# Performance work log

Measured on AMD Instinct MI355X. Metric: run time of the kernel, lower is better.

## Reference

```python
import jax, jax.numpy as jnp
import numpy as np

B, L, E, Q = 32, 2048, 512, 512

def setup_inputs() -> dict:
    key = jax.random.key(0)
    k1, k2, k3, k4, k5 = jax.random.split(key, 5)
    scale_attn = 1.0 / np.sqrt(E + Q)
    scale_v = 1.0 / np.sqrt(E)
    return {
        "embeddings": jax.random.normal(k1, (B, L, E), dtype=jnp.float32),
        "query": jax.random.normal(k2, (B, L, Q), dtype=jnp.float32),
        "W_attn": jax.random.normal(k3, (E, E + Q), dtype=jnp.float32) * scale_attn,
        "b_attn": jax.random.normal(k4, (E,), dtype=jnp.float32) * scale_attn,
        "v_w": jax.random.normal(k5, (E,), dtype=jnp.float32) * scale_v,
    }

def reference(embeddings, query, W_attn, b_attn, v_w):
    # concat along feature dim: (B, L, Q+E)
    cat = jnp.concatenate([query, embeddings], axis=2)
    # attn_layer: Linear(E+Q -> E), then tanh: (B, L, E)
    h = jnp.tanh(jnp.einsum('blf,ef->ble', cat, W_attn) + b_attn)
    # attn_v: Linear(E -> 1, no bias) -> scores (B, L)
    scores = jnp.einsum('ble,e->bl', h, v_w)
    # softmax over the sequence (dim=1 in torch)
    w = jax.nn.softmax(scores, axis=1)  # (B, L)
    # transpose to (B, 1, L) then bmm with embeddings -> (B, 1, E)
    applied = jnp.einsum('bl,ble->be', w, embeddings)[:, None, :]
    weights = w[:, None, :]
    return (applied, weights)
```

## Files before the change

kernel.cpp:

```cpp
#include <hip/hip_runtime.h>
#include <hip/hip_bf16.h>
#include <math.h>


typedef __attribute__((ext_vector_type(8))) short bf16x8;
typedef __attribute__((ext_vector_type(4))) float f32x4;

#define BDIM 32
#define LDIM 2048
#define EDIM 512
#define QDIM 512
#define KDIM 1024
#define MDIM (BDIM * LDIM)

#define BM 128
#define BN 128
#define BK 64
#define NSTEPS (KDIM / BK)

#define BAR() do { \
    asm volatile("s_waitcnt vmcnt(8) lgkmcnt(0)" ::: "memory"); \
    __builtin_amdgcn_s_barrier(); \
    __builtin_amdgcn_sched_barrier(0); \
} while (0)

__device__ __forceinline__ unsigned int pack2bf(float lo, float hi) {
    unsigned int a = __builtin_bit_cast(unsigned int, lo) + 0x8000u;
    unsigned int b = __builtin_bit_cast(unsigned int, hi) + 0x8000u;
    return __builtin_amdgcn_perm(b, a, 0x07060302);
}

__global__ __launch_bounds__(256) void convert_w_kernel(
    const float* __restrict__ W, unsigned short* __restrict__ Wsw)
{
    const int gid = blockIdx.x * 256 + threadIdx.x;
    const int n  = gid >> 7;
    const int jb = (gid & 127) * 16;
    const int sb = jb ^ ((n & 7) << 4);
    const float* src = W + (size_t)n * KDIM + (sb >> 1);
    const float4 a = *(const float4*)(src);
    const float4 c = *(const float4*)(src + 4);
    uint4 o;
    o.x = pack2bf(a.x, a.y); o.y = pack2bf(a.z, a.w);
    o.z = pack2bf(c.x, c.y); o.w = pack2bf(c.z, c.w);
    *(uint4*)((char*)Wsw + (size_t)n * 2048 + jb) = o;
}

__device__ __forceinline__ bf16x8 lds_frag(const unsigned short* buf, int row, int cb) {
    return *(const bf16x8*)((const char*)buf + row * 128 + (cb ^ ((row & 7) << 4)));
}

__device__ __forceinline__ void load_a(const float* __restrict__ emb,
                                       const float* __restrict__ query,
                                       int m0, int kstep, int arow, int acol,
                                       float4 (&r)[8])
{
    const int k0 = kstep * BK;
    const float* asrc = (k0 < QDIM) ? query : emb;
    const int koff = (k0 < QDIM) ? k0 : (k0 - QDIM);
    #pragma unroll
    for (int p = 0; p < 8; p++)
        r[p] = *(const float4*)(asrc + (size_t)(m0 + p * 16 + arow) * 512 + koff + acol);
}

__device__ __forceinline__ void write_a(unsigned short* buf, int arow, int acolb,
                                        int axor, const float4 (&r)[8])
{
    #pragma unroll
    for (int p = 0; p < 8; p++) {
        uint2 pk;
        pk.x = pack2bf(r[p].x, r[p].y);
        pk.y = pack2bf(r[p].z, r[p].w);
        *(uint2*)((char*)buf + (p * 16 + arow) * 128 + (acolb ^ axor)) = pk;
    }
}

__device__ __forceinline__ void gll_b(const unsigned short* __restrict__ Wsw,
                                      unsigned short* buf, int n0, int kstep,
                                      int brow, int bcb, int wvoff)
{
    const size_t kb = (size_t)kstep * (BK * 2);
    #pragma unroll
    for (int p = 0; p < 4; p++) {
        const char* g = (const char*)Wsw + (size_t)(n0 + p * 32 + brow) * 2048 + kb + bcb;
        __builtin_amdgcn_global_load_lds(
            (const __attribute__((address_space(1))) void*)g,
            (__attribute__((address_space(3))) void*)((char*)buf + p * 4096 + wvoff),
            16, 0, 0);
    }
}

__device__ __forceinline__ void compute_step(const unsigned short* a_,
                                             const unsigned short* b_,
                                             int wm, int wn, int ln, int quad,
                                             f32x4 (&acc)[4][4])
{
    __builtin_amdgcn_s_setprio(1);
    #pragma unroll
    for (int ks = 0; ks < 2; ks++) {
        bf16x8 af[4], bfr[4];
        #pragma unroll
        for (int i = 0; i < 4; i++) af[i] = lds_frag(a_, wm + i * 16 + ln, ks * 64 + quad * 16);
        #pragma unroll
        for (int j = 0; j < 4; j++) bfr[j] = lds_frag(b_, wn + j * 16 + ln, ks * 64 + quad * 16);
        #pragma unroll
        for (int i = 0; i < 4; i++)
            #pragma unroll
            for (int j = 0; j < 4; j++)
                acc[i][j] = __builtin_amdgcn_mfma_f32_16x16x32_bf16(af[i], bfr[j], acc[i][j], 0, 0, 0);
    }
    __builtin_amdgcn_s_setprio(0);
}

__global__ __launch_bounds__(256, 2) void scores_kernel(
    const float* __restrict__ emb, const float* __restrict__ query,
    const unsigned short* __restrict__ Wsw, const float* __restrict__ b_attn,
    const float* __restrict__ v_w, float* __restrict__ part)
{
    __shared__ __align__(16) unsigned short As[2][BM * BK];
    __shared__ __align__(16) unsigned short Bs[2][BN * BK];

    const int tid = threadIdx.x;
    const int bid = blockIdx.x;
    const int xcd = bid & 7;
    const int slot = bid >> 3;
    const int mtile = xcd * 64 + (slot >> 2);
    const int ntile = slot & 3;
    const int m0 = mtile * BM;
    const int n0 = ntile * BN;

    const int lane = tid & 63;
    const int wv = tid >> 6;
    const int wm = (wv >> 1) * 64;
    const int wn = (wv & 1) * 64;
    const int quad = lane >> 4;
    const int ln = lane & 15;

    const int arow  = tid >> 4;
    const int acol  = (tid & 15) * 4;
    const int acolb = acol * 2;
    const int axor  = (arow & 7) << 4;

    const int brow = tid >> 3;
    const int bcb  = (tid & 7) * 16;
    const int wvoff = __builtin_amdgcn_readfirstlane((tid >> 6) << 10);

    f32x4 acc[4][4];
    #pragma unroll
    for (int i = 0; i < 4; i++)
        #pragma unroll
        for (int j = 0; j < 4; j++)
            acc[i][j] = (f32x4){0.f, 0.f, 0.f, 0.f};

    float4 ra[8], rb[8];

    load_a(emb, query, m0, 0, arow, acol, ra);
    gll_b(Wsw, &Bs[0][0], n0, 0, brow, bcb, wvoff);
    load_a(emb, query, m0, 1, arow, acol, rb);
    write_a(&As[0][0], arow, acolb, axor, ra);
    BAR();

    for (int t = 0; t < NSTEPS; t += 2) {
        gll_b(Wsw, &Bs[1][0], n0, t + 1, brow, bcb, wvoff);
        {
            const int kpre = (t + 2 < NSTEPS) ? t + 2 : NSTEPS - 1;
            load_a(emb, query, m0, kpre, arow, acol, ra);
        }
        write_a(&As[1][0], arow, acolb, axor, rb);
        compute_step(&As[0][0], &Bs[0][0], wm, wn, ln, quad, acc);
        BAR();

        {
            const int kst = (t + 2 < NSTEPS) ? t + 2 : NSTEPS - 1;
            gll_b(Wsw, &Bs[0][0], n0, kst, brow, bcb, wvoff);
            const int kpre = (t + 3 < NSTEPS) ? t + 3 : NSTEPS - 1;
            load_a(emb, query, m0, kpre, arow, acol, rb);
            write_a(&As[0][0], arow, acolb, axor, ra);
        }
        compute_step(&As[1][0], &Bs[1][0], wm, wn, ln, quad, acc);
        BAR();
    }

    float bj[4], vj[4];
    #pragma unroll
    for (int j = 0; j < 4; j++) {
        const int n = n0 + wn + j * 16 + ln;
        bj[j] = b_attn[n];
        vj[j] = v_w[n];
    }
    float* redbuf = (float*)&As[0][0];
    const int half = wn >> 6;
    #pragma unroll
    for (int i = 0; i < 4; i++) {
        #pragma unroll
        for (int r = 0; r < 4; r++) {
            float s = 0.f;
            #pragma unroll
            for (int j = 0; j < 4; j++)
                s += tanhf(acc[i][j][r] + bj[j]) * vj[j];
            #pragma unroll
            for (int off = 1; off < 16; off <<= 1)
                s += __shfl_xor(s, off, 64);
            if (ln == 0)
                redbuf[half * 128 + wm + i * 16 + quad * 4 + r] = s;
        }
    }
    __syncthreads();
    if (tid < 128)
        part[(size_t)ntile * MDIM + m0 + tid] = redbuf[tid] + redbuf[128 + tid];
}

__global__ __launch_bounds__(256) void softmax_stats_kernel(
    const float* __restrict__ part, float* __restrict__ out_weights)
{
    const int b = blockIdx.x;
    const int tid = threadIdx.x;
    __shared__ float red[4];

    float sv[8];
    #pragma unroll
    for (int t = 0; t < 8; t++) {
        const size_t idx = (size_t)b * LDIM + tid + t * 256;
        float s = part[idx];
        #pragma unroll
        for (int j = 1; j < 4; j++) s += part[(size_t)j * MDIM + idx];
        sv[t] = s;
    }

    float mx = sv[0];
    #pragma unroll
    for (int t = 1; t < 8; t++) mx = fmaxf(mx, sv[t]);
    #pragma unroll
    for (int off = 1; off < 64; off <<= 1) mx = fmaxf(mx, __shfl_xor(mx, off, 64));
    if ((tid & 63) == 0) red[tid >> 6] = mx;
    __syncthreads();
    mx = fmaxf(fmaxf(red[0], red[1]), fmaxf(red[2], red[3]));

    float sm = 0.f;
    #pragma unroll
    for (int t = 0; t < 8; t++) sm += expf(sv[t] - mx);
    #pragma unroll
    for (int off = 1; off < 64; off <<= 1) sm += __shfl_xor(sm, off, 64);
    __syncthreads();
    if ((tid & 63) == 0) red[tid >> 6] = sm;
    __syncthreads();
    sm = red[0] + red[1] + red[2] + red[3];
    const float inv = 1.f / sm;

    #pragma unroll
    for (int t = 0; t < 8; t++)
        out_weights[(size_t)b * LDIM + tid + t * 256] = expf(sv[t] - mx) * inv;
}

__global__ __launch_bounds__(256) void apply_kernel(
    const float* __restrict__ emb, const float* __restrict__ w,
    float* __restrict__ out_applied)
{
    const int b = blockIdx.x >> 6;
    const int chunk = blockIdx.x & 63;
    const int l0 = chunk * 32;
    const int tid = threadIdx.x;

    __shared__ float wls[32];
    __shared__ float partial[512];

    if (tid < 32) wls[tid] = w[(size_t)b * LDIM + l0 + tid];
    __syncthreads();

    const int half = tid >> 7;
    const int cg = tid & 127;
    float4 acc = {0.f, 0.f, 0.f, 0.f};
    const float* ebase = emb + ((size_t)b * LDIM + l0 + half) * EDIM + cg * 4;
    #pragma unroll
    for (int i = 0; i < 16; i++) {
        const float4 v = *(const float4*)(ebase + (size_t)2 * i * EDIM);
        const float ww = wls[half + 2 * i];
        acc.x += ww * v.x;
        acc.y += ww * v.y;
        acc.z += ww * v.z;
        acc.w += ww * v.w;
    }
    if (half == 1) *(float4*)&partial[cg * 4] = acc;
    __syncthreads();
    if (half == 0) {
        const float4 p = *(const float4*)&partial[cg * 4];
        float* dst = out_applied + (size_t)b * EDIM + cg * 4;
        atomicAdd(dst + 0, acc.x + p.x);
        atomicAdd(dst + 1, acc.y + p.y);
        atomicAdd(dst + 2, acc.z + p.z);
        atomicAdd(dst + 3, acc.w + p.w);
    }
}

extern "C" void kernel_launch(void* const* d_in, const int* in_sizes, int n_in,
                              void* d_out, int out_size, void* d_ws, size_t ws_size,
                              hipStream_t stream) {
    const float* emb    = (const float*)d_in[0];
    const float* query  = (const float*)d_in[1];
    const float* W      = (const float*)d_in[2];
    const float* b_attn = (const float*)d_in[3];
    const float* v_w    = (const float*)d_in[4];

    float* out     = (float*)d_out;
    float* applied = out;
    float* weights = out + BDIM * EDIM;

    float* part = (float*)d_ws;
    unsigned short* Wsw = (unsigned short*)((char*)d_ws + (size_t)4 * MDIM * 4);

    hipMemsetAsync(applied, 0, (size_t)BDIM * EDIM * sizeof(float), stream);

    convert_w_kernel<<<256, 256, 0, stream>>>(W, Wsw);

    scores_kernel<<<2048, 256, 0, stream>>>(emb, query, Wsw, b_attn, v_w, part);

    softmax_stats_kernel<<<32, 256, 0, stream>>>(part, weights);

    apply_kernel<<<2048, 256, 0, stream>>>(emb, weights, applied);
}
```

Before: 392.1 us.

## Load GEMM fragments directly from global memory into registers, bypassing LDS

The LDS-staged, double-buffered tiling of A and B is replaced by per-wave loads straight into registers, with two register chunk buffers alternating in a loop. The W conversion no longer swizzles and writes plain row-major bf16. This removes LDS traffic and barriers, but each wave now fetches its own A and B fragments with no sharing across waves. That raises global and L2 traffic, and the small strided loads leave less latency hiding.

```diff
diff --git a/kernel.cpp b/kernel.cpp
--- a/kernel.cpp
+++ b/kernel.cpp
@@ -15,14 +15,7 @@
 
 #define BM 128
 #define BN 128
-#define BK 64
-#define NSTEPS (KDIM / BK)
-
-#define BAR() do { \
-    asm volatile("s_waitcnt vmcnt(8) lgkmcnt(0)" ::: "memory"); \
-    __builtin_amdgcn_s_barrier(); \
-    __builtin_amdgcn_sched_barrier(0); \
-} while (0)
+#define NCHUNK 32
 
 __device__ __forceinline__ unsigned int pack2bf(float lo, float hi) {
     unsigned int a = __builtin_bit_cast(unsigned int, lo) + 0x8000u;
@@ -30,95 +23,68 @@
     return __builtin_amdgcn_perm(b, a, 0x07060302);
 }
 
+__device__ __forceinline__ bf16x8 pack_frag(const float4& lo, const float4& hi) {
+    union { unsigned int u[4]; bf16x8 v; } r;
+    r.u[0] = pack2bf(lo.x, lo.y);
+    r.u[1] = pack2bf(lo.z, lo.w);
+    r.u[2] = pack2bf(hi.x, hi.y);
+    r.u[3] = pack2bf(hi.z, hi.w);
+    return r.v;
+}
+
 __global__ __launch_bounds__(256) void convert_w_kernel(
-    const float* __restrict__ W, unsigned short* __restrict__ Wsw)
+    const float* __restrict__ W, unsigned short* __restrict__ Wbf)
 {
     const int gid = blockIdx.x * 256 + threadIdx.x;
-    const int n  = gid >> 7;
-    const int jb = (gid & 127) * 16;
-    const int sb = jb ^ ((n & 7) << 4);
-    const float* src = W + (size_t)n * KDIM + (sb >> 1);
+    const float* src = W + (size_t)gid * 8;
     const float4 a = *(const float4*)(src);
     const float4 c = *(const float4*)(src + 4);
     uint4 o;
     o.x = pack2bf(a.x, a.y); o.y = pack2bf(a.z, a.w);
     o.z = pack2bf(c.x, c.y); o.w = pack2bf(c.z, c.w);
-    *(uint4*)((char*)Wsw + (size_t)n * 2048 + jb) = o;
-}
-
-__device__ __forceinline__ bf16x8 lds_frag(const unsigned short* buf, int row, int cb) {
-    return *(const bf16x8*)((const char*)buf + row * 128 + (cb ^ ((row & 7) << 4)));
-}
-
-__device__ __forceinline__ void load_a(const float* __restrict__ emb,
-                                       const float* __restrict__ query,
-                                       int m0, int kstep, int arow, int acol,
-                                       float4 (&r)[8])
-{
-    const int k0 = kstep * BK;
-    const float* asrc = (k0 < QDIM) ? query : emb;
-    const int koff = (k0 < QDIM) ? k0 : (k0 - QDIM);
-    #pragma unroll
-    for (int p = 0; p < 8; p++)
-        r[p] = *(const float4*)(asrc + (size_t)(m0 + p * 16 + arow) * 512 + koff + acol);
-}
-
-__device__ __forceinline__ void write_a(unsigned short* buf, int arow, int acolb,
-                                        int axor, const float4 (&r)[8])
-{
-    #pragma unroll
-    for (int p = 0; p < 8; p++) {
-        uint2 pk;
-        pk.x = pack2bf(r[p].x, r[p].y);
-        pk.y = pack2bf(r[p].z, r[p].w);
-        *(uint2*)((char*)buf + (p * 16 + arow) * 128 + (acolb ^ axor)) = pk;
-    }
-}
-
-__device__ __forceinline__ void gll_b(const unsigned short* __restrict__ Wsw,
-                                      unsigned short* buf, int n0, int kstep,
-                                      int brow, int bcb, int wvoff)
-{
-    const size_t kb = (size_t)kstep * (BK * 2);
-    #pragma unroll
-    for (int p = 0; p < 4; p++) {
-        const char* g = (const char*)Wsw + (size_t)(n0 + p * 32 + brow) * 2048 + kb + bcb;
-        __builtin_amdgcn_global_load_lds(
-            (const __attribute__((address_space(1))) void*)g,
-            (__attribute__((address_space(3))) void*)((char*)buf + p * 4096 + wvoff),
-            16, 0, 0);
-    }
-}
-
-__device__ __forceinline__ void compute_step(const unsigned short* a_,
-                                             const unsigned short* b_,
-                                             int wm, int wn, int ln, int quad,
-                                             f32x4 (&acc)[4][4])
-{
-    __builtin_amdgcn_s_setprio(1);
-    #pragma unroll
-    for (int ks = 0; ks < 2; ks++) {
-        bf16x8 af[4], bfr[4];
-        #pragma unroll
-        for (int i = 0; i < 4; i++) af[i] = lds_frag(a_, wm + i * 16 + ln, ks * 64 + quad * 16);
-        #pragma unroll
-        for (int j = 0; j < 4; j++) bfr[j] = lds_frag(b_, wn + j * 16 + ln, ks * 64 + quad * 16);
-        #pragma unroll
-        for (int i = 0; i < 4; i++)
-            #pragma unroll
-            for (int j = 0; j < 4; j++)
-                acc[i][j] = __builtin_amdgcn_mfma_f32_16x16x32_bf16(af[i], bfr[j], acc[i][j], 0, 0, 0);
-    }
-    __builtin_amdgcn_s_setprio(0);
-}
-
-__global__ __launch_bounds__(256, 2) void scores_kernel(
+    *(uint4*)(Wbf + (size_t)gid * 8) = o;
+}
+
+__device__ __forceinline__ void load_chunk(
     const float* __restrict__ emb, const float* __restrict__ query,
-    const unsigned short* __restrict__ Wsw, const float* __restrict__ b_attn,
+    const unsigned short* __restrict__ Wbf,
+    int arow0, int brow0, int ln, int quad, int c,
+    float4 (&a0)[4], float4 (&a1)[4], bf16x8 (&bfr)[4])
+{
+    const int kq = c * 32 + quad * 8;
+    const float* asrc = (kq < QDIM) ? query : emb;
+    const int koff = (kq < QDIM) ? kq : (kq - QDIM);
+    #pragma unroll
+    for (int i = 0; i < 4; i++) {
+        const float* p = asrc + (size_t)(arow0 + i * 16) * 512 + koff;
+        a0[i] = *(const float4*)p;
+        a1[i] = *(const float4*)(p + 4);
+    }
+    #pragma unroll
+    for (int j = 0; j < 4; j++)
+        bfr[j] = *(const bf16x8*)(Wbf + (size_t)(brow0 + j * 16) * 1024 + c * 32 + quad * 8);
+}
+
+__device__ __forceinline__ void compute_chunk(
+    const float4 (&a0)[4], const float4 (&a1)[4], const bf16x8 (&bfr)[4],
+    f32x4 (&acc)[4][4])
+{
+    bf16x8 af[4];
+    #pragma unroll
+    for (int i = 0; i < 4; i++) af[i] = pack_frag(a0[i], a1[i]);
+    #pragma unroll
+    for (int i = 0; i < 4; i++)
+        #pragma unroll
+        for (int j = 0; j < 4; j++)
+            acc[i][j] = __builtin_amdgcn_mfma_f32_16x16x32_bf16(af[i], bfr[j], acc[i][j], 0, 0, 0);
+}
+
+__global__ __launch_bounds__(256) void scores_kernel(
+    const float* __restrict__ emb, const float* __restrict__ query,
+    const unsigned short* __restrict__ Wbf, const float* __restrict__ b_attn,
     const float* __restrict__ v_w, float* __restrict__ part)
 {
-    __shared__ __align__(16) unsigned short As[2][BM * BK];
-    __shared__ __align__(16) unsigned short Bs[2][BN * BK];
+    __shared__ float redbuf[256];
 
     const int tid = threadIdx.x;
     const int bid = blockIdx.x;
@@ -136,14 +102,8 @@
     const int quad = lane >> 4;
     const int ln = lane & 15;
 
-    const int arow  = tid >> 4;
-    const int acol  = (tid & 15) * 4;
-    const int acolb = acol * 2;
-    const int axor  = (arow & 7) << 4;
-
-    const int brow = tid >> 3;
-    const int bcb  = (tid & 7) * 16;
-    const int wvoff = __builtin_amdgcn_readfirstlane((tid >> 6) << 10);
+    const int arow0 = m0 + wm + ln;
+    const int brow0 = n0 + wn + ln;
 
     f32x4 acc[4][4];
     #pragma unroll
@@ -152,33 +112,18 @@
         for (int j = 0; j < 4; j++)
             acc[i][j] = (f32x4){0.f, 0.f, 0.f, 0.f};
 
-    float4 ra[8], rb[8];
-
-    load_a(emb, query, m0, 0, arow, acol, ra);
-    gll_b(Wsw, &Bs[0][0], n0, 0, brow, bcb, wvoff);
-    load_a(emb, query, m0, 1, arow, acol, rb);
-    write_a(&As[0][0], arow, acolb, axor, ra);
-    BAR();
-
-    for (int t = 0; t < NSTEPS; t += 2) {
-        gll_b(Wsw, &Bs[1][0], n0, t + 1, brow, bcb, wvoff);
-        {
-            const int kpre = (t + 2 < NSTEPS) ? t + 2 : NSTEPS - 1;
-            load_a(emb, query, m0, kpre, arow, acol, ra);
-        }
-        write_a(&As[1][0], arow, acolb, axor, rb);
-        compute_step(&As[0][0], &Bs[0][0], wm, wn, ln, quad, acc);
-        BAR();
-
-        {
-            const int kst = (t + 2 < NSTEPS) ? t + 2 : NSTEPS - 1;
-            gll_b(Wsw, &Bs[0][0], n0, kst, brow, bcb, wvoff);
-            const int kpre = (t + 3 < NSTEPS) ? t + 3 : NSTEPS - 1;
-            load_a(emb, query, m0, kpre, arow, acol, rb);
-            write_a(&As[0][0], arow, acolb, axor, ra);
-        }
-        compute_step(&As[1][0], &Bs[1][0], wm, wn, ln, quad, acc);
-        BAR();
+    float4 a0A[4], a1A[4], a0B[4], a1B[4];
+    bf16x8 bA[4], bB[4];
+
+    load_chunk(emb, query, Wbf, arow0, brow0, ln, quad, 0, a0A, a1A, bA);
+
+    #pragma unroll 1
+    for (int c = 0; c < NCHUNK; c += 2) {
+        load_chunk(emb, query, Wbf, arow0, brow0, ln, quad, c + 1, a0B, a1B, bB);
+        compute_chunk(a0A, a1A, bA, acc);
+        if (c + 2 < NCHUNK)
+            load_chunk(emb, query, Wbf, arow0, brow0, ln, quad, c + 2, a0A, a1A, bA);
+        compute_chunk(a0B, a1B, bB, acc);
     }
 
     float bj[4], vj[4];
@@ -188,7 +133,6 @@
         bj[j] = b_attn[n];
         vj[j] = v_w[n];
     }
-    float* redbuf = (float*)&As[0][0];
     const int half = wn >> 6;
     #pragma unroll
     for (int i = 0; i < 4; i++) {
@@ -306,13 +250,13 @@
     float* weights = out + BDIM * EDIM;
 
     float* part = (float*)d_ws;
-    unsigned short* Wsw = (unsigned short*)((char*)d_ws + (size_t)4 * MDIM * 4);
+    unsigned short* Wbf = (unsigned short*)((char*)d_ws + (size_t)4 * MDIM * 4);
 
     hipMemsetAsync(applied, 0, (size_t)BDIM * EDIM * sizeof(float), stream);
 
-    convert_w_kernel<<<256, 256, 0, stream>>>(W, Wsw);
-
-    scores_kernel<<<2048, 256, 0, stream>>>(emb, query, Wsw, b_attn, v_w, part);
+    convert_w_kernel<<<256, 256, 0, stream>>>(W, Wbf);
+
+    scores_kernel<<<2048, 256, 0, stream>>>(emb, query, Wbf, b_attn, v_w, part);
 
     softmax_stats_kernel<<<32, 256, 0, stream>>>(part, weights);
 
```

After: 581.5 us. +48.3%, slower.

## Use 512-thread GEMM blocks with 8 waves and simpler double-buffer pipeline

Applied to the files above, without the earlier changes.

Runs the scores GEMM with 512 threads per block, so each of 8 waves computes a 64x32 sub-tile. This halves per-thread accumulators and load registers and aims for higher occupancy. The custom vmcnt barrier and the two-step-ahead register prefetch are replaced by plain __syncthreads with one-step-ahead loads, which may expose more memory latency. The apply kernel also processes 64 rows per block with half as many blocks, reducing atomic traffic.

```diff
diff --git a/kernel.cpp b/kernel.cpp
--- a/kernel.cpp
+++ b/kernel.cpp
@@ -17,12 +17,6 @@
 #define BN 128
 #define BK 64
 #define NSTEPS (KDIM / BK)
-
-#define BAR() do { \
-    asm volatile("s_waitcnt vmcnt(8) lgkmcnt(0)" ::: "memory"); \
-    __builtin_amdgcn_s_barrier(); \
-    __builtin_amdgcn_sched_barrier(0); \
-} while (0)
 
 __device__ __forceinline__ unsigned int pack2bf(float lo, float hi) {
     unsigned int a = __builtin_bit_cast(unsigned int, lo) + 0x8000u;
@@ -53,25 +47,25 @@
 __device__ __forceinline__ void load_a(const float* __restrict__ emb,
                                        const float* __restrict__ query,
                                        int m0, int kstep, int arow, int acol,
-                                       float4 (&r)[8])
+                                       float4 (&r)[4])
 {
     const int k0 = kstep * BK;
     const float* asrc = (k0 < QDIM) ? query : emb;
     const int koff = (k0 < QDIM) ? k0 : (k0 - QDIM);
     #pragma unroll
-    for (int p = 0; p < 8; p++)
-        r[p] = *(const float4*)(asrc + (size_t)(m0 + p * 16 + arow) * 512 + koff + acol);
+    for (int p = 0; p < 4; p++)
+        r[p] = *(const float4*)(asrc + (size_t)(m0 + p * 32 + arow) * 512 + koff + acol);
 }
 
 __device__ __forceinline__ void write_a(unsigned short* buf, int arow, int acolb,
-                                        int axor, const float4 (&r)[8])
-{
-    #pragma unroll
-    for (int p = 0; p < 8; p++) {
+                                        int axor, const float4 (&r)[4])
+{
+    #pragma unroll
+    for (int p = 0; p < 4; p++) {
         uint2 pk;
         pk.x = pack2bf(r[p].x, r[p].y);
         pk.y = pack2bf(r[p].z, r[p].w);
-        *(uint2*)((char*)buf + (p * 16 + arow) * 128 + (acolb ^ axor)) = pk;
+        *(uint2*)((char*)buf + (p * 32 + arow) * 128 + (acolb ^ axor)) = pk;
     }
 }
 
@@ -81,11 +75,11 @@
 {
     const size_t kb = (size_t)kstep * (BK * 2);
     #pragma unroll
-    for (int p = 0; p < 4; p++) {
-        const char* g = (const char*)Wsw + (size_t)(n0 + p * 32 + brow) * 2048 + kb + bcb;
+    for (int p = 0; p < 2; p++) {
+        const char* g = (const char*)Wsw + (size_t)(n0 + p * 64 + brow) * 2048 + kb + bcb;
         __builtin_amdgcn_global_load_lds(
             (const __attribute__((address_space(1))) void*)g,
-            (__attribute__((address_space(3))) void*)((char*)buf + p * 4096 + wvoff),
+            (__attribute__((address_space(3))) void*)((char*)buf + p * 8192 + wvoff),
             16, 0, 0);
     }
 }
@@ -93,26 +87,26 @@
 __device__ __forceinline__ void compute_step(const unsigned short* a_,
                                              const unsigned short* b_,
                                              int wm, int wn, int ln, int quad,
-                                             f32x4 (&acc)[4][4])
+                                             f32x4 (&acc)[4][2])
 {
     __builtin_amdgcn_s_setprio(1);
     #pragma unroll
     for (int ks = 0; ks < 2; ks++) {
-        bf16x8 af[4], bfr[4];
+        bf16x8 af[4], bfr[2];
         #pragma unroll
         for (int i = 0; i < 4; i++) af[i] = lds_frag(a_, wm + i * 16 + ln, ks * 64 + quad * 16);
         #pragma unroll
-        for (int j = 0; j < 4; j++) bfr[j] = lds_frag(b_, wn + j * 16 + ln, ks * 64 + quad * 16);
+        for (int j = 0; j < 2; j++) bfr[j] = lds_frag(b_, wn + j * 16 + ln, ks * 64 + quad * 16);
         #pragma unroll
         for (int i = 0; i < 4; i++)
             #pragma unroll
-            for (int j = 0; j < 4; j++)
+            for (int j = 0; j < 2; j++)
                 acc[i][j] = __builtin_amdgcn_mfma_f32_16x16x32_bf16(af[i], bfr[j], acc[i][j], 0, 0, 0);
     }
     __builtin_amdgcn_s_setprio(0);
 }
 
-__global__ __launch_bounds__(256, 2) void scores_kernel(
+__global__ __launch_bounds__(512, 4) void scores_kernel(
     const float* __restrict__ emb, const float* __restrict__ query,
     const unsigned short* __restrict__ Wsw, const float* __restrict__ b_attn,
     const float* __restrict__ v_w, float* __restrict__ part)
@@ -131,8 +125,8 @@
 
     const int lane = tid & 63;
     const int wv = tid >> 6;
-    const int wm = (wv >> 1) * 64;
-    const int wn = (wv & 1) * 64;
+    const int wm = (wv >> 2) * 64;
+    const int wn = (wv & 3) * 32;
     const int quad = lane >> 4;
     const int ln = lane & 15;
 
@@ -143,71 +137,71 @@
 
     const int brow = tid >> 3;
     const int bcb  = (tid & 7) * 16;
-    const int wvoff = __builtin_amdgcn_readfirstlane((tid >> 6) << 10);
-
-    f32x4 acc[4][4];
+    const int wvoff = __builtin_amdgcn_readfirstlane(wv << 10);
+
+    f32x4 acc[4][2];
     #pragma unroll
     for (int i = 0; i < 4; i++)
         #pragma unroll
-        for (int j = 0; j < 4; j++)
+        for (int j = 0; j < 2; j++)
             acc[i][j] = (f32x4){0.f, 0.f, 0.f, 0.f};
 
-    float4 ra[8], rb[8];
-
+    float4 ra[4];
+
+    gll_b(Wsw, &Bs[0][0], n0, 0, brow, bcb, wvoff);
     load_a(emb, query, m0, 0, arow, acol, ra);
-    gll_b(Wsw, &Bs[0][0], n0, 0, brow, bcb, wvoff);
-    load_a(emb, query, m0, 1, arow, acol, rb);
     write_a(&As[0][0], arow, acolb, axor, ra);
-    BAR();
-
+    __syncthreads();
+
+    #pragma unroll 1
     for (int t = 0; t < NSTEPS; t += 2) {
         gll_b(Wsw, &Bs[1][0], n0, t + 1, brow, bcb, wvoff);
-        {
-            const int kpre = (t + 2 < NSTEPS) ? t + 2 : NSTEPS - 1;
-            load_a(emb, query, m0, kpre, arow, acol, ra);
-        }
-        write_a(&As[1][0], arow, acolb, axor, rb);
+        load_a(emb, query, m0, t + 1, arow, acol, ra);
         compute_step(&As[0][0], &Bs[0][0], wm, wn, ln, quad, acc);
-        BAR();
-
-        {
-            const int kst = (t + 2 < NSTEPS) ? t + 2 : NSTEPS - 1;
-            gll_b(Wsw, &Bs[0][0], n0, kst, brow, bcb, wvoff);
-            const int kpre = (t + 3 < NSTEPS) ? t + 3 : NSTEPS - 1;
-            load_a(emb, query, m0, kpre, arow, acol, rb);
-            write_a(&As[0][0], arow, acolb, axor, ra);
+        write_a(&As[1][0], arow, acolb, axor, ra);
+        __syncthreads();
+
+        if (t + 2 < NSTEPS) {
+            gll_b(Wsw, &Bs[0][0], n0, t + 2, brow, bcb, wvoff);
+            load_a(emb, query, m0, t + 2, arow, acol, ra);
         }
         compute_step(&As[1][0], &Bs[1][0], wm, wn, ln, quad, acc);
-        BAR();
-    }
-
-    float bj[4], vj[4];
-    #pragma unroll
-    for (int j = 0; j < 4; j++) {
+        if (t + 2 < NSTEPS)
+            write_a(&As[0][0], arow, acolb, axor, ra);
+        __syncthreads();
+    }
+
+    float bj[2], vj[2];
+    #pragma unroll
+    for (int j = 0; j < 2; j++) {
         const int n = n0 + wn + j * 16 + ln;
         bj[j] = b_attn[n];
         vj[j] = v_w[n];
     }
     float* redbuf = (float*)&As[0][0];
-    const int half = wn >> 6;
     #pragma unroll
     for (int i = 0; i < 4; i++) {
         #pragma unroll
         for (int r = 0; r < 4; r++) {
             float s = 0.f;
             #pragma unroll
-            for (int j = 0; j < 4; j++)
+            for (int j = 0; j < 2; j++)
                 s += tanhf(acc[i][j][r] + bj[j]) * vj[j];
             #pragma unroll
             for (int off = 1; off < 16; off <<= 1)
                 s += __shfl_xor(s, off, 64);
             if (ln == 0)
-                redbuf[half * 128 + wm + i * 16 + quad * 4 + r] = s;
+                redbuf[wv * 64 + i * 16 + quad * 4 + r] = s;
         }
     }
     __syncthreads();
-    if (tid < 128)
-        part[(size_t)ntile * MDIM + m0 + tid] = redbuf[tid] + redbuf[128 + tid];
+    if (tid < 128) {
+        const int h = tid >> 6;
+        const int r = tid & 63;
+        const float s = redbuf[(h * 4 + 0) * 64 + r] + redbuf[(h * 4 + 1) * 64 + r]
+                      + redbuf[(h * 4 + 2) * 64 + r] + redbuf[(h * 4 + 3) * 64 + r];
+        part[(size_t)ntile * MDIM + m0 + tid] = s;
+    }
 }
 
 __global__ __launch_bounds__(256) void softmax_stats_kernel(
@@ -256,23 +250,23 @@
     const float* __restrict__ emb, const float* __restrict__ w,
     float* __restrict__ out_applied)
 {
-    const int b = blockIdx.x >> 6;
-    const int chunk = blockIdx.x & 63;
-    const int l0 = chunk * 32;
+    const int b = blockIdx.x >> 5;
+    const int chunk = blockIdx.x & 31;
+    const int l0 = chunk * 64;
     const int tid = threadIdx.x;
 
-    __shared__ float wls[32];
+    __shared__ float wls[64];
     __shared__ float partial[512];
 
-    if (tid < 32) wls[tid] = w[(size_t)b * LDIM + l0 + tid];
+    if (tid < 64) wls[tid] = w[(size_t)b * LDIM + l0 + tid];
     __syncthreads();
 
     const int half = tid >> 7;
     const int cg = tid & 127;
     float4 acc = {0.f, 0.f, 0.f, 0.f};
     const float* ebase = emb + ((size_t)b * LDIM + l0 + half) * EDIM + cg * 4;
-    #pragma unroll
-    for (int i = 0; i < 16; i++) {
+    #pragma unroll 8
+    for (int i = 0; i < 32; i++) {
         const float4 v = *(const float4*)(ebase + (size_t)2 * i * EDIM);
         const float ww = wls[half + 2 * i];
         acc.x += ww * v.x;
@@ -312,9 +306,9 @@
 
     convert_w_kernel<<<256, 256, 0, stream>>>(W, Wsw);
 
-    scores_kernel<<<2048, 256, 0, stream>>>(emb, query, Wsw, b_attn, v_w, part);
+    scores_kernel<<<2048, 512, 0, stream>>>(emb, query, Wsw, b_attn, v_w, part);
 
     softmax_stats_kernel<<<32, 256, 0, stream>>>(part, weights);
 
-    apply_kernel<<<2048, 256, 0, stream>>>(emb, weights, applied);
-}
+    apply_kernel<<<1024, 256, 0, stream>>>(emb, weights, applied);
+}
```

Measured after the change: 385.4 us. No clear change (-1.7%).
